# Performance work log

Measured on AMD Instinct MI355X. Metric: run time of the kernel, lower is better.

Reference implementation:

```python
import jax, jax.numpy as jnp
import numpy as np
import math

HIDDEN = 2048
HEADS = 16
HEAD_DIM = HIDDEN // HEADS
MAX_SEQ = 2048
BATCH = 2
SEQ = 2048


def _rope_tables(seq_len, dim):
    inv_freq = 1.0 / (10000.0 ** (np.arange(0, dim, 2, dtype=np.float32) / dim))
    t = np.arange(seq_len, dtype=np.float32)
    freqs = np.einsum('i,j->ij', t, inv_freq)  # [S, dim/2]
    emb = np.concatenate([freqs, freqs], axis=-1)  # [S, dim]
    return jnp.asarray(np.cos(emb)), jnp.asarray(np.sin(emb))


def setup_inputs() -> dict:
    key = jax.random.key(0)
    ks = jax.random.split(key, 5)
    s = 1.0 / math.sqrt(HIDDEN)
    x = jax.random.normal(ks[0], (BATCH, SEQ, HIDDEN), dtype=jnp.float32)
    Wq = jax.random.normal(ks[1], (HIDDEN, HIDDEN), dtype=jnp.float32) * s
    Wk = jax.random.normal(ks[2], (HIDDEN, HIDDEN), dtype=jnp.float32) * s
    Wv = jax.random.normal(ks[3], (HIDDEN, HIDDEN), dtype=jnp.float32) * s
    Wo = jax.random.normal(ks[4], (HIDDEN, HIDDEN), dtype=jnp.float32) * s
    return {"x": x, "Wq": Wq, "Wk": Wk, "Wv": Wv, "Wo": Wo}


def _rotate_half(t):
    t1, t2 = t[..., : t.shape[-1] // 2], t[..., t.shape[-1] // 2 :]
    return jnp.concatenate([-t2, t1], axis=-1)


def reference(x, Wq, Wk, Wv, Wo):
    b, s, _ = x.shape
    # nn.Linear: y = x @ W.T
    def proj(W):
        return jnp.einsum('bsd,hd->bsh', x, W).reshape(b, s, HEADS, HEAD_DIM).transpose(0, 2, 1, 3)
    q, k, v = proj(Wq), proj(Wk), proj(Wv)  # [b, H, s, hd]
    cos, sin = _rope_tables(s, HEAD_DIM)    # [s, hd]
    cos = cos[None, None]
    sin = sin[None, None]
    q = q * cos + _rotate_half(q) * sin
    k = k * cos + _rotate_half(k) * sin
    scale = 1.0 / math.sqrt(HEAD_DIM)
    scores = jnp.einsum('bhqd,bhkd->bhqk', q, k) * scale
    causal = jnp.triu(jnp.ones((s, s), dtype=bool), k=1)
    scores = jnp.where(causal[None, None], -jnp.inf, scores)
    attn = jax.nn.softmax(scores, axis=-1)
    out = jnp.einsum('bhqk,bhkd->bhqd', attn, v)
    out = out.transpose(0, 2, 1, 3).reshape(b, s, HIDDEN)
    return jnp.einsum('bsd,hd->bsh', out, Wo)
```

## Files before the change

kernel.cpp:

```cpp
#include <hip/hip_runtime.h>
#include <stdint.h>


#define SCALE_Q 0.08838834764831845f

typedef short bf16x8 __attribute__((ext_vector_type(8)));
typedef float f32x4 __attribute__((ext_vector_type(4)));
typedef unsigned short u16x4v __attribute__((ext_vector_type(4)));
typedef unsigned short u16x8v __attribute__((ext_vector_type(8)));

__device__ __forceinline__ unsigned short f2bf(float f) {
  unsigned u = __float_as_uint(f);
  return (unsigned short)((u + 0x7FFFu + ((u >> 16) & 1u)) >> 16);
}
__device__ __forceinline__ float bf2f(unsigned short h) {
  return __uint_as_float(((unsigned)h) << 16);
}
__device__ __forceinline__ void gld16(void* lds, const void* g) {
  __builtin_amdgcn_global_load_lds(
      (const __attribute__((address_space(1))) unsigned int*)g,
      (__attribute__((address_space(3))) unsigned int*)lds, 16, 0, 0);
}

__global__ __launch_bounds__(256) void cvt_all(
    const float* __restrict__ x, const float* __restrict__ wq,
    const float* __restrict__ wk, const float* __restrict__ wv,
    const float* __restrict__ wo,
    unsigned short* __restrict__ xb, unsigned short* __restrict__ wqkv,
    unsigned short* __restrict__ wob) {
  int r = blockIdx.y;
  size_t i = ((size_t)blockIdx.x * 256 + threadIdx.x) * 8;
  const float* src; unsigned short* dst; size_t n;
  if (r == 0)      { src = x;  dst = xb;             n = 8388608; }
  else if (r == 1) { src = wq; dst = wqkv;           n = 4194304; }
  else if (r == 2) { src = wk; dst = wqkv + 4194304; n = 4194304; }
  else if (r == 3) { src = wv; dst = wqkv + 8388608; n = 4194304; }
  else             { src = wo; dst = wob;            n = 4194304; }
  if (i >= n) return;
  float4 a = *(const float4*)(src + i);
  float4 b = *(const float4*)(src + i + 4);
  u16x8v o;
  o[0] = f2bf(a.x); o[1] = f2bf(a.y); o[2] = f2bf(a.z); o[3] = f2bf(a.w);
  o[4] = f2bf(b.x); o[5] = f2bf(b.y); o[6] = f2bf(b.z); o[7] = f2bf(b.w);
  *(u16x8v*)(dst + i) = o;
}

__global__ __launch_bounds__(256) void rope_table(float* __restrict__ ct, float* __restrict__ st) {
  int id = blockIdx.x * 256 + threadIdx.x;
  int s = id >> 6, j = id & 63;
  float inv = __powf(10000.0f, -(float)j * (1.0f / 64.0f));
  float a = (float)s * inv;
  ct[id] = __cosf(a);
  st[id] = __sinf(a);
}

__global__ __launch_bounds__(512, 2) void gemm_qk(
    const unsigned short* __restrict__ A, const unsigned short* __restrict__ B,
    unsigned short* __restrict__ Qo, unsigned short* __restrict__ Ko, int Kd) {
  __shared__ unsigned short As[4][128 * 64];
  __shared__ unsigned short Bs[4][128 * 64];
  const int t = threadIdx.x;
  const int lane = t & 63, w = t >> 6;
  const int g = lane >> 4, c15 = lane & 15;
  const int wm = w >> 2, wn = w & 3;

  const int chunk = (int)blockIdx.x & 7;
  const int idx = (int)blockIdx.x >> 3;
  const int row = idx & 15;
  const int col = chunk * 2 + (idx >> 4);
  const int brow = row * 256, bcol = col * 256;

  const int l = t >> 3;
  const int lg = (t & 7) ^ (l & 7);
  const unsigned short* srcA = A + (size_t)(brow + l + ((lg >> 2) << 7)) * Kd + (lg & 3) * 8;
  const unsigned short* srcB = B + (size_t)(bcol + l + ((lg >> 2) << 7)) * Kd + (lg & 3) * 8;

  auto stage = [&](int kt) {
    const int buf = kt & 3;
    const unsigned short* a = srcA + kt * 32;
    const unsigned short* b = srcB + kt * 32;
    gld16((char*)As[buf] + t * 16, a);
    gld16((char*)As[buf] + 8192 + t * 16, a + (size_t)64 * Kd);
    gld16((char*)Bs[buf] + t * 16, b);
    gld16((char*)Bs[buf] + 8192 + t * 16, b + (size_t)64 * Kd);
  };

  const int aoff = c15 * 128 + ((((wm << 2) | g) ^ (c15 & 7)) << 4);
  const int boff = ((wn & 1) << 13) + c15 * 128 + (((((wn >> 1) << 2) | g) ^ (c15 & 7)) << 4);

  f32x4 zero4 = {0.f, 0.f, 0.f, 0.f};
  f32x4 acc[8][4];
#pragma unroll
  for (int a_ = 0; a_ < 8; ++a_)
#pragma unroll
    for (int b_ = 0; b_ < 4; ++b_) acc[a_][b_] = zero4;

  const int nk = Kd >> 5;
  stage(0); stage(1); stage(2);
  asm volatile("s_waitcnt vmcnt(8)" ::: "memory");
  __builtin_amdgcn_s_barrier();

  for (int kt = 0; kt < nk; ++kt) {
    const char* ab = (const char*)As[kt & 3];
    const char* bb = (const char*)Bs[kt & 3];
    bf16x8 bfv[4], af0[4], af1[4];
#pragma unroll
    for (int nj = 0; nj < 4; ++nj) bfv[nj] = *(const bf16x8*)(bb + boff + nj * 2048);
#pragma unroll
    for (int mi = 0; mi < 4; ++mi) af0[mi] = *(const bf16x8*)(ab + aoff + mi * 2048);
    __builtin_amdgcn_sched_barrier(0);
#pragma unroll
    for (int mi = 0; mi < 4; ++mi) af1[mi] = *(const bf16x8*)(ab + aoff + (mi + 4) * 2048);
    if (kt + 3 < nk) stage(kt + 3);
    asm volatile("s_waitcnt lgkmcnt(4)" ::: "memory");
    __builtin_amdgcn_sched_barrier(0);
    __builtin_amdgcn_s_setprio(1);
#pragma unroll
    for (int mi = 0; mi < 4; ++mi)
#pragma unroll
      for (int nj = 0; nj < 4; ++nj)
        acc[mi][nj] = __builtin_amdgcn_mfma_f32_16x16x32_bf16(
            af0[mi], bfv[nj], acc[mi][nj], 0, 0, 0);
    __builtin_amdgcn_s_setprio(0);
    asm volatile("s_waitcnt lgkmcnt(0)" ::: "memory");
    __builtin_amdgcn_sched_barrier(0);
    __builtin_amdgcn_s_setprio(1);
#pragma unroll
    for (int mi = 0; mi < 4; ++mi)
#pragma unroll
      for (int nj = 0; nj < 4; ++nj)
        acc[mi + 4][nj] = __builtin_amdgcn_mfma_f32_16x16x32_bf16(
            af1[mi], bfv[nj], acc[mi + 4][nj], 0, 0, 0);
    __builtin_amdgcn_s_setprio(0);
    if (kt + 3 < nk) {
      asm volatile("s_waitcnt vmcnt(8)" ::: "memory");
    } else if (kt + 2 < nk) {
      asm volatile("s_waitcnt vmcnt(4)" ::: "memory");
    } else if (kt + 1 < nk) {
      asm volatile("s_waitcnt vmcnt(0)" ::: "memory");
    }
    __builtin_amdgcn_s_barrier();
  }

#pragma unroll
  for (int mi = 0; mi < 8; ++mi) {
#pragma unroll
    for (int nj = 0; nj < 4; ++nj) {
      f32x4 v = acc[mi][nj];
      int row0 = brow + wm * 128 + mi * 16 + g * 4;
      int colc = bcol + wn * 64 + nj * 16 + c15;
      int which = colc >> 11;
      int hc = colc & 2047;
      int bh = ((row0 >> 11) << 4) + (hc >> 7);
      int d = hc & 127, s0 = row0 & 2047;
      unsigned short* dst =
          (which ? Ko : Qo) + ((size_t)bh * 2048 + s0) * 128 + d;
#pragma unroll
      for (int i2 = 0; i2 < 4; ++i2) dst[(size_t)i2 * 128] = f2bf(v[i2]);
    }
  }
}

__global__ __launch_bounds__(512, 2) void gemm_v(
    const unsigned short* __restrict__ A, const unsigned short* __restrict__ B,
    unsigned short* __restrict__ Vt, int Kd) {
  __shared__ unsigned short As[4][64 * 64];
  __shared__ unsigned short Bs[4][128 * 64];
  const int t = threadIdx.x;
  const int lane = t & 63, w = t >> 6;
  const int g = lane >> 4, c15 = lane & 15;
  const int wm = w >> 2, wn = w & 3;

  const int chunk = (int)blockIdx.x & 7;
  const int idx = (int)blockIdx.x >> 3;
  const int row = chunk * 4 + (idx >> 3);
  const int col = idx & 7;
  const int brow = row * 128, bcol = col * 256;

  const int l = t >> 3;
  const int lg = (t & 7) ^ (l & 7);
  const unsigned short* srcA = A + (size_t)(brow + l + ((lg >> 2) << 6)) * Kd + (lg & 3) * 8;
  const unsigned short* srcB = B + (size_t)(bcol + l + ((lg >> 2) << 7)) * Kd + (lg & 3) * 8;

  auto stage = [&](int kt) {
    const int buf = kt & 3;
    const unsigned short* a = srcA + kt * 32;
    const unsigned short* b = srcB + kt * 32;
    gld16((char*)As[buf] + t * 16, a);
    gld16((char*)Bs[buf] + t * 16, b);
    gld16((char*)Bs[buf] + 8192 + t * 16, b + (size_t)64 * Kd);
  };

  const int aoff = c15 * 128 + ((((wm << 2) | g) ^ (c15 & 7)) << 4);
  const int boff = ((wn & 1) << 13) + c15 * 128 + (((((wn >> 1) << 2) | g) ^ (c15 & 7)) << 4);

  f32x4 zero4 = {0.f, 0.f, 0.f, 0.f};
  f32x4 acc[4][4];
#pragma unroll
  for (int a_ = 0; a_ < 4; ++a_)
#pragma unroll
    for (int b_ = 0; b_ < 4; ++b_) acc[a_][b_] = zero4;

  const int nk = Kd >> 5;
  stage(0); stage(1); stage(2);
  asm volatile("s_waitcnt vmcnt(6)" ::: "memory");
  __builtin_amdgcn_s_barrier();

  for (int kt = 0; kt < nk; ++kt) {
    const char* ab = (const char*)As[kt & 3];
    const char* bb = (const char*)Bs[kt & 3];
    bf16x8 bfv[4], af0[2], af1[2];
#pragma unroll
    for (int nj = 0; nj < 4; ++nj) bfv[nj] = *(const bf16x8*)(bb + boff + nj * 2048);
#pragma unroll
    for (int mi = 0; mi < 2; ++mi) af0[mi] = *(const bf16x8*)(ab + aoff + mi * 2048);
    __builtin_amdgcn_sched_barrier(0);
#pragma unroll
    for (int mi = 0; mi < 2; ++mi) af1[mi] = *(const bf16x8*)(ab + aoff + (mi + 2) * 2048);
    if (kt + 3 < nk) stage(kt + 3);
    asm volatile("s_waitcnt lgkmcnt(2)" ::: "memory");
    __builtin_amdgcn_sched_barrier(0);
    __builtin_amdgcn_s_setprio(1);
#pragma unroll
    for (int mi = 0; mi < 2; ++mi)
#pragma unroll
      for (int nj = 0; nj < 4; ++nj)
        acc[mi][nj] = __builtin_amdgcn_mfma_f32_16x16x32_bf16(
            af0[mi], bfv[nj], acc[mi][nj], 0, 0, 0);
    __builtin_amdgcn_s_setprio(0);
    asm volatile("s_waitcnt lgkmcnt(0)" ::: "memory");
    __builtin_amdgcn_sched_barrier(0);
    __builtin_amdgcn_s_setprio(1);
#pragma unroll
    for (int mi = 0; mi < 2; ++mi)
#pragma unroll
      for (int nj = 0; nj < 4; ++nj)
        acc[mi + 2][nj] = __builtin_amdgcn_mfma_f32_16x16x32_bf16(
            af1[mi], bfv[nj], acc[mi + 2][nj], 0, 0, 0);
    __builtin_amdgcn_s_setprio(0);
    if (kt + 3 < nk) {
      asm volatile("s_waitcnt vmcnt(6)" ::: "memory");
    } else if (kt + 3 == nk) {
      asm volatile("s_waitcnt vmcnt(3)" ::: "memory");
    } else if (kt + 2 == nk) {
      asm volatile("s_waitcnt vmcnt(0)" ::: "memory");
    }
    __builtin_amdgcn_s_barrier();
  }

#pragma unroll
  for (int mi = 0; mi < 4; ++mi) {
#pragma unroll
    for (int nj = 0; nj < 4; ++nj) {
      f32x4 v = acc[mi][nj];
      int row0 = brow + wm * 64 + mi * 16 + g * 4;
      int colc = bcol + wn * 64 + nj * 16 + c15;
      int bh = ((row0 >> 11) << 4) + (colc >> 7);
      int d = colc & 127, s0 = row0 & 2047;
      u16x4v pk;
      pk[0] = f2bf(v[0]); pk[1] = f2bf(v[1]); pk[2] = f2bf(v[2]); pk[3] = f2bf(v[3]);
      *(u16x4v*)(Vt + ((size_t)bh * 128 + d) * 2048 + s0) = pk;
    }
  }
}

__global__ __launch_bounds__(256) void gemm_bt(
    const unsigned short* __restrict__ A, const unsigned short* __restrict__ B,
    float* __restrict__ C, int N, int Kd) {
  __shared__ unsigned short As[128 * 64];
  __shared__ unsigned short Bs[128 * 64];
  const int t = threadIdx.x;
  const int lane = t & 63, w = t >> 6;
  const int g = lane >> 4, c15 = lane & 15;
  const int wr = w >> 1, wc = w & 1;
  const int brow = blockIdx.y * 128, bcol = blockIdx.x * 128;
  const int srow = t >> 3;
  const int ssl = (t & 7) ^ (srow & 7);
  const unsigned short* pA = A + (size_t)(brow + srow) * Kd + ssl * 8;
  const unsigned short* pB = B + (size_t)(bcol + srow) * Kd + ssl * 8;

  int aoff[4][2], boff[4][2];
#pragma unroll
  for (int mi = 0; mi < 4; ++mi)
#pragma unroll
    for (int kk = 0; kk < 2; ++kk) {
      int arow = wr * 64 + mi * 16 + c15;
      int bcolr = wc * 64 + mi * 16 + c15;
      int p = (kk * 4 + g) ^ (c15 & 7);
      aoff[mi][kk] = arow * 128 + (p << 4);
      boff[mi][kk] = bcolr * 128 + (p << 4);
    }
  f32x4 zero4 = {0.f, 0.f, 0.f, 0.f};
  f32x4 acc[4][4];
#pragma unroll
  for (int a_ = 0; a_ < 4; ++a_)
#pragma unroll
    for (int b_ = 0; b_ < 4; ++b_) acc[a_][b_] = zero4;

  const int nk = Kd >> 6;
  for (int kt = 0; kt < nk; ++kt) {
    const unsigned short* a0 = pA + kt * 64;
    const unsigned short* b0 = pB + kt * 64;
#pragma unroll
    for (int c = 0; c < 4; ++c) {
      gld16((char*)As + c * 4096 + t * 16, a0 + (size_t)c * 32 * Kd);
      gld16((char*)Bs + c * 4096 + t * 16, b0 + (size_t)c * 32 * Kd);
    }
    __syncthreads();
    bf16x8 af[4][2], bfv[4][2];
#pragma unroll
    for (int mi = 0; mi < 4; ++mi)
#pragma unroll
      for (int kk = 0; kk < 2; ++kk) {
        af[mi][kk] = *(const bf16x8*)((const char*)As + aoff[mi][kk]);
        bfv[mi][kk] = *(const bf16x8*)((const char*)Bs + boff[mi][kk]);
      }
#pragma unroll
    for (int mi = 0; mi < 4; ++mi)
#pragma unroll
      for (int nj = 0; nj < 4; ++nj)
#pragma unroll
        for (int kk = 0; kk < 2; ++kk)
          acc[mi][nj] = __builtin_amdgcn_mfma_f32_16x16x32_bf16(
              af[mi][kk], bfv[nj][kk], acc[mi][nj], 0, 0, 0);
    __syncthreads();
  }
#pragma unroll
  for (int mi = 0; mi < 4; ++mi)
#pragma unroll
    for (int nj = 0; nj < 4; ++nj) {
      f32x4 v = acc[mi][nj];
      int row0 = brow + wr * 64 + mi * 16 + g * 4;
      int colc = bcol + wc * 64 + nj * 16 + c15;
#pragma unroll
      for (int i = 0; i < 4; ++i) C[(size_t)(row0 + i) * N + colc] = v[i];
    }
}

__global__ __launch_bounds__(256) void rope_apply(
    unsigned short* __restrict__ Q, unsigned short* __restrict__ K,
    const float* __restrict__ ct, const float* __restrict__ st) {
  int id = blockIdx.x * 256 + threadIdx.x;
  int o = id & 7;
  int s = (id >> 3) & 2047;
  int bh = id >> 14;
  size_t base = ((size_t)bh * 2048 + s) * 128 + o * 8;
  u16x8v qlo = *(u16x8v*)(Q + base), qhi = *(u16x8v*)(Q + base + 64);
  u16x8v klo = *(u16x8v*)(K + base), khi = *(u16x8v*)(K + base + 64);
  const float* cp = ct + s * 64 + o * 8;
  const float* sp = st + s * 64 + o * 8;
#pragma unroll
  for (int j = 0; j < 8; ++j) {
    float c = cp[j], sn = sp[j];
    float ql = bf2f(qlo[j]), qh = bf2f(qhi[j]);
    qlo[j] = f2bf((ql * c - qh * sn) * SCALE_Q);
    qhi[j] = f2bf((qh * c + ql * sn) * SCALE_Q);
    float kl = bf2f(klo[j]), kh = bf2f(khi[j]);
    klo[j] = f2bf(kl * c - kh * sn);
    khi[j] = f2bf(kh * c + kl * sn);
  }
  *(u16x8v*)(Q + base) = qlo; *(u16x8v*)(Q + base + 64) = qhi;
  *(u16x8v*)(K + base) = klo; *(u16x8v*)(K + base + 64) = khi;
}

__global__ __launch_bounds__(512) void attn_fwd(
    const unsigned short* __restrict__ Qg, const unsigned short* __restrict__ Kg,
    const unsigned short* __restrict__ Vtg, unsigned short* __restrict__ Og) {
  __shared__ unsigned short Ks[2][64 * 128];
  __shared__ unsigned short Vs[2][128 * 64];
  __shared__ unsigned short Pl[8][16 * 88];
  const int t = threadIdx.x;
  const int lane = t & 63, w = t >> 6;
  const int g = lane >> 4, c15 = lane & 15;
  const int pair = blockIdx.x;
  const int bh = blockIdx.y;
  const int b = bh >> 4, h = bh & 15;

  const int ksrow = t >> 4;
  const int kssl = (t & 15) ^ (ksrow & 15);
  const unsigned short* kp = Kg + ((size_t)bh * 2048 + ksrow) * 128 + kssl * 8;
  const int vsrow = t >> 3;
  const int vssl = (t & 7) ^ (vsrow & 7);
  const unsigned short* vp = Vtg + ((size_t)bh * 128 + vsrow) * 2048 + vssl * 8;

  auto stageTile = [&](int buf, int tkv) {
    gld16((char*)Ks[buf] + t * 16, kp + (size_t)(tkv * 64) * 128);
    gld16((char*)Ks[buf] + 8192 + t * 16, kp + (size_t)(tkv * 64 + 32) * 128);
    gld16((char*)Vs[buf] + t * 16, vp + tkv * 64);
    gld16((char*)Vs[buf] + 8192 + t * 16, vp + (size_t)64 * 2048 + tkv * 64);
  };

  f32x4 zero4 = {0.f, 0.f, 0.f, 0.f};
  f32x4 o[8];
  float mrow[4], lrow[4];
  bf16x8 qf[4];

  auto loadQ = [&](int qb) {
    const unsigned short* qp =
        Qg + ((size_t)bh * 2048 + qb * 128 + w * 16 + c15) * 128 + g * 8;
#pragma unroll
    for (int kf = 0; kf < 4; ++kf) qf[kf] = *(const bf16x8*)(qp + kf * 32);
#pragma unroll
    for (int db = 0; db < 8; ++db) o[db] = zero4;
#pragma unroll
    for (int i = 0; i < 4; ++i) { mrow[i] = -1e30f; lrow[i] = 0.f; }
  };

  auto computeTile = [&](int buf, int qb, int tkv) {
    const int qrow = qb * 128 + w * 16;
    f32x4 sv[4];
    __builtin_amdgcn_s_setprio(1);
#pragma unroll
    for (int cb = 0; cb < 4; ++cb) {
      f32x4 z = zero4;
#pragma unroll
      for (int kf = 0; kf < 4; ++kf) {
        int rowk = cb * 16 + c15;
        int p = (kf * 4 + g) ^ c15;
        bf16x8 kfr = *(const bf16x8*)((const char*)Ks[buf] + rowk * 256 + p * 16);
        z = __builtin_amdgcn_mfma_f32_16x16x32_bf16(qf[kf], kfr, z, 0, 0, 0);
      }
      sv[cb] = z;
    }
    __builtin_amdgcn_s_setprio(0);
    if (tkv >= 2 * qb) {
#pragma unroll
      for (int cb = 0; cb < 4; ++cb)
#pragma unroll
        for (int i = 0; i < 4; ++i) {
          int colk = tkv * 64 + cb * 16 + c15;
          int rq = qrow + g * 4 + i;
          if (colk > rq) sv[cb][i] = -1e30f;
        }
    }
    float pmx[4];
#pragma unroll
    for (int i = 0; i < 4; ++i)
      pmx[i] = fmaxf(fmaxf(sv[0][i], sv[1][i]), fmaxf(sv[2][i], sv[3][i]));
#pragma unroll
    for (int dd = 1; dd < 16; dd <<= 1)
#pragma unroll
      for (int i = 0; i < 4; ++i) pmx[i] = fmaxf(pmx[i], __shfl_xor(pmx[i], dd));
    int grow = 0;
#pragma unroll
    for (int i = 0; i < 4; ++i) grow |= (pmx[i] > mrow[i] + 8.0f) ? 1 : 0;
    if (__any(grow)) {
#pragma unroll
      for (int i = 0; i < 4; ++i) {
        float nm = fmaxf(mrow[i], pmx[i]);
        float sc = __expf(mrow[i] - nm);
        mrow[i] = nm;
        lrow[i] *= sc;
#pragma unroll
        for (int db = 0; db < 8; ++db) o[db][i] *= sc;
      }
    }
    float psum[4] = {0.f, 0.f, 0.f, 0.f};
#pragma unroll
    for (int cb = 0; cb < 4; ++cb)
#pragma unroll
      for (int i = 0; i < 4; ++i) {
        float e = __expf(sv[cb][i] - mrow[i]);
        sv[cb][i] = e;
        psum[i] += e;
      }
#pragma unroll
    for (int dd = 1; dd < 16; dd <<= 1)
#pragma unroll
      for (int i = 0; i < 4; ++i) psum[i] += __shfl_xor(psum[i], dd);
#pragma unroll
    for (int i = 0; i < 4; ++i) lrow[i] += psum[i];

    unsigned short* pw = &Pl[w][0];
#pragma unroll
    for (int cb = 0; cb < 4; ++cb)
#pragma unroll
      for (int i = 0; i < 4; ++i)
        pw[(g * 4 + i) * 88 + cb * 16 + c15] = f2bf(sv[cb][i]);
    bf16x8 pf[2];
#pragma unroll
    for (int kb = 0; kb < 2; ++kb)
      pf[kb] = *(const bf16x8*)((const char*)pw + c15 * 176 + kb * 64 + g * 16);

    __builtin_amdgcn_s_setprio(1);
#pragma unroll
    for (int db = 0; db < 8; ++db) {
#pragma unroll
      for (int kb = 0; kb < 2; ++kb) {
        int rowv = db * 16 + c15;
        int p = (kb * 4 + g) ^ (c15 & 7);
        bf16x8 vfr = *(const bf16x8*)((const char*)Vs[buf] + rowv * 128 + p * 16);
        o[db] = __builtin_amdgcn_mfma_f32_16x16x32_bf16(pf[kb], vfr, o[db], 0, 0, 0);
      }
    }
    __builtin_amdgcn_s_setprio(0);
  };

  auto writeO = [&](int qb) {
    float linv[4];
#pragma unroll
    for (int i = 0; i < 4; ++i) linv[i] = 1.0f / lrow[i];
#pragma unroll
    for (int db = 0; db < 8; ++db)
#pragma unroll
      for (int i = 0; i < 4; ++i) {
        int q = qb * 128 + w * 16 + g * 4 + i;
        Og[((size_t)(b * 2048 + q)) * 2048 + h * 128 + db * 16 + c15] =
            f2bf(o[db][i] * linv[i]);
      }
  };

  const int qbA = pair, qbB = 15 - pair;
  const int ntA = 2 * qbA + 2, ntB = 2 * qbB + 2;
  int cur = 0;

  stageTile(0, 0);
  loadQ(qbA);
  for (int tkv = 0; tkv < ntA; ++tkv) {
    if (tkv + 1 < ntA) stageTile(cur ^ 1, tkv + 1);
    else               stageTile(cur ^ 1, 0);
    asm volatile("s_waitcnt vmcnt(4)" ::: "memory");
    __builtin_amdgcn_s_barrier();
    computeTile(cur, qbA, tkv);
    __builtin_amdgcn_s_barrier();
    cur ^= 1;
  }
  writeO(qbA);
  loadQ(qbB);
  for (int tkv = 0; tkv < ntB; ++tkv) {
    if (tkv + 1 < ntB) {
      stageTile(cur ^ 1, tkv + 1);
      asm volatile("s_waitcnt vmcnt(4)" ::: "memory");
    } else {
      asm volatile("s_waitcnt vmcnt(0)" ::: "memory");
    }
    __builtin_amdgcn_s_barrier();
    computeTile(cur, qbB, tkv);
    __builtin_amdgcn_s_barrier();
    cur ^= 1;
  }
  writeO(qbB);
}

extern "C" void kernel_launch(void* const* d_in, const int* in_sizes, int n_in,
                              void* d_out, int out_size, void* d_ws, size_t ws_size,
                              hipStream_t stream) {
  const float* x  = (const float*)d_in[0];
  const float* Wq = (const float*)d_in[1];
  const float* Wk = (const float*)d_in[2];
  const float* Wv = (const float*)d_in[3];
  const float* Wo = (const float*)d_in[4];
  char* p = (char*)d_ws;
  unsigned short* xb    = (unsigned short*)p;
  unsigned short* wqkvb = (unsigned short*)(p + 16777216);
  unsigned short* wob   = (unsigned short*)(p + 41943040);
  unsigned short* Qb    = (unsigned short*)(p + 50331648);
  unsigned short* Kb    = (unsigned short*)(p + 67108864);
  unsigned short* Vt    = (unsigned short*)(p + 83886080);
  float* ctab           = (float*)(p + 100663296);
  float* stab           = (float*)(p + 101187584);
  unsigned short* Ao = xb;

  cvt_all<<<dim3(4096, 5), 256, 0, stream>>>(x, Wq, Wk, Wv, Wo, xb, wqkvb, wob);
  rope_table<<<512, 256, 0, stream>>>(ctab, stab);
  gemm_qk<<<256, 512, 0, stream>>>(xb, wqkvb, Qb, Kb, 2048);
  gemm_v<<<256, 512, 0, stream>>>(xb, wqkvb + (size_t)4096 * 2048, Vt, 2048);
  rope_apply<<<2048, 256, 0, stream>>>(Qb, Kb, ctab, stab);
  attn_fwd<<<dim3(8, 32), 512, 0, stream>>>(Qb, Kb, Vt, Ao);
  gemm_bt<<<dim3(16, 32), 256, 0, stream>>>(Ao, wob, (float*)d_out, 2048, 2048);
}
```

Measured before the change: 278.2 us.

## Rewrite attention with 32x32x16 MFMA and four 32-row waves per block

The attention kernel switches from 16x16x32 to 32x32x16 bf16 MFMA, computing S transposed so each lane owns one query row. This turns the 16-lane shuffle reductions for row max and sum into a single xor-32 shuffle. Blocks drop from 8 waves to 4, with each wave covering 32 query rows, and the K/V staging is reissued as four loads each, with the wait counts adjusted to match. The larger MFMA tiles are meant to cut LDS fragment traffic and softmax overhead, at the cost of higher register pressure and fewer waves per block to hide latency.

```diff
diff --git a/kernel.cpp b/kernel.cpp
--- a/kernel.cpp
+++ b/kernel.cpp
@@ -6,8 +6,11 @@
 
 typedef short bf16x8 __attribute__((ext_vector_type(8)));
 typedef float f32x4 __attribute__((ext_vector_type(4)));
+typedef float f32x16 __attribute__((ext_vector_type(16)));
 typedef unsigned short u16x4v __attribute__((ext_vector_type(4)));
 typedef unsigned short u16x8v __attribute__((ext_vector_type(8)));
+
+#define MFMA32 __builtin_amdgcn_mfma_f32_32x32x16_bf16
 
 __device__ __forceinline__ unsigned short f2bf(float f) {
   unsigned u = __float_as_uint(f);
@@ -363,15 +366,15 @@
   *(u16x8v*)(K + base) = klo; *(u16x8v*)(K + base + 64) = khi;
 }
 
-__global__ __launch_bounds__(512) void attn_fwd(
+__global__ __launch_bounds__(256) void attn_fwd(
     const unsigned short* __restrict__ Qg, const unsigned short* __restrict__ Kg,
     const unsigned short* __restrict__ Vtg, unsigned short* __restrict__ Og) {
   __shared__ unsigned short Ks[2][64 * 128];
   __shared__ unsigned short Vs[2][128 * 64];
-  __shared__ unsigned short Pl[8][16 * 88];
+  __shared__ unsigned short Pl[4][32 * 72];
   const int t = threadIdx.x;
   const int lane = t & 63, w = t >> 6;
-  const int g = lane >> 4, c15 = lane & 15;
+  const int q31 = lane & 31, hi = lane >> 5;
   const int pair = blockIdx.x;
   const int bh = blockIdx.y;
   const int b = bh >> 4, h = bh & 15;
@@ -384,129 +387,127 @@
   const unsigned short* vp = Vtg + ((size_t)bh * 128 + vsrow) * 2048 + vssl * 8;
 
   auto stageTile = [&](int buf, int tkv) {
-    gld16((char*)Ks[buf] + t * 16, kp + (size_t)(tkv * 64) * 128);
-    gld16((char*)Ks[buf] + 8192 + t * 16, kp + (size_t)(tkv * 64 + 32) * 128);
-    gld16((char*)Vs[buf] + t * 16, vp + tkv * 64);
-    gld16((char*)Vs[buf] + 8192 + t * 16, vp + (size_t)64 * 2048 + tkv * 64);
+#pragma unroll
+    for (int g2 = 0; g2 < 4; ++g2)
+      gld16((char*)Ks[buf] + g2 * 4096 + t * 16, kp + (size_t)(tkv * 64 + g2 * 16) * 128);
+#pragma unroll
+    for (int g2 = 0; g2 < 4; ++g2)
+      gld16((char*)Vs[buf] + g2 * 4096 + t * 16,
+            vp + (size_t)(g2 * 32) * 2048 + tkv * 64);
   };
 
-  f32x4 zero4 = {0.f, 0.f, 0.f, 0.f};
-  f32x4 o[8];
-  float mrow[4], lrow[4];
-  bf16x8 qf[4];
+  f32x16 o[4];
+  float mrow, lrow;
+  bf16x8 qf[8];
 
   auto loadQ = [&](int qb) {
     const unsigned short* qp =
-        Qg + ((size_t)bh * 2048 + qb * 128 + w * 16 + c15) * 128 + g * 8;
-#pragma unroll
-    for (int kf = 0; kf < 4; ++kf) qf[kf] = *(const bf16x8*)(qp + kf * 32);
-#pragma unroll
-    for (int db = 0; db < 8; ++db) o[db] = zero4;
-#pragma unroll
-    for (int i = 0; i < 4; ++i) { mrow[i] = -1e30f; lrow[i] = 0.f; }
+        Qg + ((size_t)bh * 2048 + qb * 128 + w * 32 + q31) * 128 + hi * 8;
+#pragma unroll
+    for (int kf = 0; kf < 8; ++kf) qf[kf] = *(const bf16x8*)(qp + kf * 16);
+#pragma unroll
+    for (int db = 0; db < 4; ++db)
+#pragma unroll
+      for (int r = 0; r < 16; ++r) o[db][r] = 0.f;
+    mrow = -1e30f; lrow = 0.f;
   };
 
   auto computeTile = [&](int buf, int qb, int tkv) {
-    const int qrow = qb * 128 + w * 16;
-    f32x4 sv[4];
+    f32x16 st0, st1;
+#pragma unroll
+    for (int r = 0; r < 16; ++r) { st0[r] = 0.f; st1[r] = 0.f; }
+    const int krow0 = q31, krow1 = 32 + q31;
+    const int ksw = q31 & 15;
     __builtin_amdgcn_s_setprio(1);
 #pragma unroll
-    for (int cb = 0; cb < 4; ++cb) {
-      f32x4 z = zero4;
-#pragma unroll
-      for (int kf = 0; kf < 4; ++kf) {
-        int rowk = cb * 16 + c15;
-        int p = (kf * 4 + g) ^ c15;
-        bf16x8 kfr = *(const bf16x8*)((const char*)Ks[buf] + rowk * 256 + p * 16);
-        z = __builtin_amdgcn_mfma_f32_16x16x32_bf16(qf[kf], kfr, z, 0, 0, 0);
+    for (int kf = 0; kf < 8; ++kf) {
+      int sl = ((kf * 2 + hi) ^ ksw) * 16;
+      bf16x8 k0 = *(const bf16x8*)((const char*)Ks[buf] + krow0 * 256 + sl);
+      bf16x8 k1 = *(const bf16x8*)((const char*)Ks[buf] + krow1 * 256 + sl);
+      st0 = MFMA32(k0, qf[kf], st0, 0, 0, 0);
+      st1 = MFMA32(k1, qf[kf], st1, 0, 0, 0);
+    }
+    __builtin_amdgcn_s_setprio(0);
+    const int qg = qb * 128 + w * 32 + q31;
+    if (tkv >= 2 * qb) {
+#pragma unroll
+      for (int r = 0; r < 16; ++r) {
+        int k0i = tkv * 64 + (r & 3) + 8 * (r >> 2) + 4 * hi;
+        if (k0i > qg) st0[r] = -1e30f;
+        if (k0i + 32 > qg) st1[r] = -1e30f;
       }
-      sv[cb] = z;
-    }
-    __builtin_amdgcn_s_setprio(0);
-    if (tkv >= 2 * qb) {
-#pragma unroll
-      for (int cb = 0; cb < 4; ++cb)
-#pragma unroll
-        for (int i = 0; i < 4; ++i) {
-          int colk = tkv * 64 + cb * 16 + c15;
-          int rq = qrow + g * 4 + i;
-          if (colk > rq) sv[cb][i] = -1e30f;
-        }
-    }
-    float pmx[4];
-#pragma unroll
-    for (int i = 0; i < 4; ++i)
-      pmx[i] = fmaxf(fmaxf(sv[0][i], sv[1][i]), fmaxf(sv[2][i], sv[3][i]));
-#pragma unroll
-    for (int dd = 1; dd < 16; dd <<= 1)
-#pragma unroll
-      for (int i = 0; i < 4; ++i) pmx[i] = fmaxf(pmx[i], __shfl_xor(pmx[i], dd));
-    int grow = 0;
-#pragma unroll
-    for (int i = 0; i < 4; ++i) grow |= (pmx[i] > mrow[i] + 8.0f) ? 1 : 0;
-    if (__any(grow)) {
-#pragma unroll
-      for (int i = 0; i < 4; ++i) {
-        float nm = fmaxf(mrow[i], pmx[i]);
-        float sc = __expf(mrow[i] - nm);
-        mrow[i] = nm;
-        lrow[i] *= sc;
-#pragma unroll
-        for (int db = 0; db < 8; ++db) o[db][i] *= sc;
+    }
+    float mx[8];
+#pragma unroll
+    for (int r = 0; r < 8; ++r)
+      mx[r] = fmaxf(fmaxf(st0[r], st0[r + 8]), fmaxf(st1[r], st1[r + 8]));
+#pragma unroll
+    for (int r = 0; r < 4; ++r) mx[r] = fmaxf(mx[r], mx[r + 4]);
+    float pmx = fmaxf(fmaxf(mx[0], mx[1]), fmaxf(mx[2], mx[3]));
+    pmx = fmaxf(pmx, __shfl_xor(pmx, 32));
+    if (pmx > mrow + 8.0f) {
+      float sc = __expf(mrow - pmx);
+      mrow = pmx;
+      lrow *= sc;
+#pragma unroll
+      for (int db = 0; db < 4; ++db) o[db] *= sc;
+    }
+    float s4[4] = {0.f, 0.f, 0.f, 0.f};
+#pragma unroll
+    for (int r = 0; r < 16; ++r) {
+      float e = __expf(st0[r] - mrow); st0[r] = e; s4[r & 3] += e;
+    }
+#pragma unroll
+    for (int r = 0; r < 16; ++r) {
+      float e = __expf(st1[r] - mrow); st1[r] = e; s4[r & 3] += e;
+    }
+    float ps = (s4[0] + s4[1]) + (s4[2] + s4[3]);
+    ps += __shfl_xor(ps, 32);
+    lrow += ps;
+    char* pw = (char*)Pl + w * (32 * 144) + q31 * 144 + hi * 8;
+#pragma unroll
+    for (int rq = 0; rq < 4; ++rq) {
+      u16x4v a, c;
+#pragma unroll
+      for (int j = 0; j < 4; ++j) {
+        a[j] = f2bf(st0[rq * 4 + j]);
+        c[j] = f2bf(st1[rq * 4 + j]);
       }
-    }
-    float psum[4] = {0.f, 0.f, 0.f, 0.f};
-#pragma unroll
-    for (int cb = 0; cb < 4; ++cb)
-#pragma unroll
-      for (int i = 0; i < 4; ++i) {
-        float e = __expf(sv[cb][i] - mrow[i]);
-        sv[cb][i] = e;
-        psum[i] += e;
-      }
-#pragma unroll
-    for (int dd = 1; dd < 16; dd <<= 1)
-#pragma unroll
-      for (int i = 0; i < 4; ++i) psum[i] += __shfl_xor(psum[i], dd);
-#pragma unroll
-    for (int i = 0; i < 4; ++i) lrow[i] += psum[i];
-
-    unsigned short* pw = &Pl[w][0];
-#pragma unroll
-    for (int cb = 0; cb < 4; ++cb)
-#pragma unroll
-      for (int i = 0; i < 4; ++i)
-        pw[(g * 4 + i) * 88 + cb * 16 + c15] = f2bf(sv[cb][i]);
-    bf16x8 pf[2];
-#pragma unroll
-    for (int kb = 0; kb < 2; ++kb)
-      pf[kb] = *(const bf16x8*)((const char*)pw + c15 * 176 + kb * 64 + g * 16);
-
+      *(u16x4v*)(pw + rq * 16) = a;
+      *(u16x4v*)(pw + 64 + rq * 16) = c;
+    }
+    const char* pr = (const char*)Pl + w * (32 * 144) + q31 * 144;
+    bf16x8 pa[4];
+#pragma unroll
+    for (int kfp = 0; kfp < 4; ++kfp)
+      pa[kfp] = *(const bf16x8*)(pr + kfp * 32 + hi * 16);
     __builtin_amdgcn_s_setprio(1);
 #pragma unroll
-    for (int db = 0; db < 8; ++db) {
-#pragma unroll
-      for (int kb = 0; kb < 2; ++kb) {
-        int rowv = db * 16 + c15;
-        int p = (kb * 4 + g) ^ (c15 & 7);
-        bf16x8 vfr = *(const bf16x8*)((const char*)Vs[buf] + rowv * 128 + p * 16);
-        o[db] = __builtin_amdgcn_mfma_f32_16x16x32_bf16(pf[kb], vfr, o[db], 0, 0, 0);
+    for (int db = 0; db < 4; ++db) {
+      int vrow = db * 32 + q31;
+      int vsw = vrow & 7;
+#pragma unroll
+      for (int kfp = 0; kfp < 4; ++kfp) {
+        int sl = ((kfp * 2 + hi) ^ vsw) * 16;
+        bf16x8 vfr = *(const bf16x8*)((const char*)Vs[buf] + vrow * 128 + sl);
+        o[db] = MFMA32(vfr, pa[kfp], o[db], 0, 0, 0);
       }
     }
     __builtin_amdgcn_s_setprio(0);
   };
 
   auto writeO = [&](int qb) {
-    float linv[4];
-#pragma unroll
-    for (int i = 0; i < 4; ++i) linv[i] = 1.0f / lrow[i];
-#pragma unroll
-    for (int db = 0; db < 8; ++db)
-#pragma unroll
-      for (int i = 0; i < 4; ++i) {
-        int q = qb * 128 + w * 16 + g * 4 + i;
-        Og[((size_t)(b * 2048 + q)) * 2048 + h * 128 + db * 16 + c15] =
-            f2bf(o[db][i] * linv[i]);
+    float linv = 1.0f / lrow;
+    int qg = qb * 128 + w * 32 + q31;
+    unsigned short* ob = Og + ((size_t)(b * 2048 + qg)) * 2048 + h * 128;
+#pragma unroll
+    for (int db = 0; db < 4; ++db)
+#pragma unroll
+      for (int rq = 0; rq < 4; ++rq) {
+        u16x4v pk;
+#pragma unroll
+        for (int j = 0; j < 4; ++j) pk[j] = f2bf(o[db][rq * 4 + j] * linv);
+        *(u16x4v*)(ob + db * 32 + 8 * rq + 4 * hi) = pk;
       }
   };
 
@@ -519,7 +520,7 @@
   for (int tkv = 0; tkv < ntA; ++tkv) {
     if (tkv + 1 < ntA) stageTile(cur ^ 1, tkv + 1);
     else               stageTile(cur ^ 1, 0);
-    asm volatile("s_waitcnt vmcnt(4)" ::: "memory");
+    asm volatile("s_waitcnt vmcnt(8)" ::: "memory");
     __builtin_amdgcn_s_barrier();
     computeTile(cur, qbA, tkv);
     __builtin_amdgcn_s_barrier();
@@ -530,7 +531,7 @@
   for (int tkv = 0; tkv < ntB; ++tkv) {
     if (tkv + 1 < ntB) {
       stageTile(cur ^ 1, tkv + 1);
-      asm volatile("s_waitcnt vmcnt(4)" ::: "memory");
+      asm volatile("s_waitcnt vmcnt(8)" ::: "memory");
     } else {
       asm volatile("s_waitcnt vmcnt(0)" ::: "memory");
     }
@@ -566,6 +567,6 @@
   gemm_qk<<<256, 512, 0, stream>>>(xb, wqkvb, Qb, Kb, 2048);
   gemm_v<<<256, 512, 0, stream>>>(xb, wqkvb + (size_t)4096 * 2048, Vt, 2048);
   rope_apply<<<2048, 256, 0, stream>>>(Qb, Kb, ctab, stab);
-  attn_fwd<<<dim3(8, 32), 512, 0, stream>>>(Qb, Kb, Vt, Ao);
+  attn_fwd<<<dim3(8, 32), 256, 0, stream>>>(Qb, Kb, Vt, Ao);
   gemm_bt<<<dim3(16, 32), 256, 0, stream>>>(Ao, wob, (float*)d_out, 2048, 2048);
 }
```

Measured after the change: 279.5 us. No clear change (+0.5%).
